# Kernel tuning notes

Hardware: AMD Instinct MI355X
Metric: run time of the kernel (lower is better)

Reference implementation:

```python
import jax, jax.numpy as jnp
import numpy as np

J = 24          # SMPL_NR_JOINTS
H = 24          # hidden_dim
D_IN = 3        # input_dim (xyz)
SMPL_PARENTS = [-1, 0, 0, 0, 1, 2, 3, 4, 5, 6, 7, 8, 9, 9, 9, 12, 13, 14, 16, 17, 18, 19, 20, 21]

def _build_A():
    # undirected kinematic tree + self loops, row-normalized (mean aggregation)
    M = np.zeros((J, J), np.float32)
    for child, parent in enumerate(SMPL_PARENTS):
        if parent >= 0:
            M[child, parent] = 1.0
            M[parent, child] = 1.0
    M += np.eye(J, dtype=np.float32)
    M /= M.sum(axis=1, keepdims=True)
    return jnp.asarray(M)

A_NORM = _build_A()  # [J, J]

def setup_inputs() -> dict:
    key = jax.random.key(0)
    ks = jax.random.split(key, 12)
    B, S, T = 2048, 24, 24
    g = lambda k, shape, s=0.1: jax.random.normal(k, shape, dtype=jnp.float32) * s
    return {
        "src": g(ks[0], (B, S, J, D_IN), 1.0),
        "tgt": g(ks[1], (B, T, J, D_IN), 1.0),
        "We": g(ks[2], (H, D_IN)), "be": jnp.zeros((H,), jnp.float32),
        # gate order: 0=i, 1=f, 2=c, 3=o
        "Wxl": g(ks[3], (4, H, H)), "bxl": jnp.zeros((4, H), jnp.float32),
        "Wxr": g(ks[4], (4, H, H)),
        "Whl": g(ks[5], (4, H, H)), "bhl": jnp.zeros((4, H), jnp.float32),
        "Whr": g(ks[6], (4, H, H)),
        "wg": g(ks[7], (3, H)),   # peephole weights for i, f, o
        "bg": jnp.zeros((4, H), jnp.float32),
        "Wd": g(ks[8], (D_IN * J, H * J)), "bd": jnp.zeros((D_IN * J,), jnp.float32),
    }

def _gconv(x, Wl, bl, Wr):
    # x: [B, J, D]; mean-aggregate over fixed 24-node graph, then l(agg) + r(x)
    agg = jnp.einsum('ij,bjd->bid', A_NORM, x)
    return agg @ Wl.T + bl + x @ Wr.T

def _cell(X, h, c, Wxl, bxl, Wxr, Whl, bhl, Whr, wg, bg):
    gx = lambda g: _gconv(X, Wxl[g], bxl[g], Wxr[g])
    gh = lambda g: _gconv(h, Whl[g], bhl[g], Whr[g])
    i = jax.nn.sigmoid(gx(0) + gh(0) + wg[0] * c + bg[0])
    f = jax.nn.sigmoid(gx(1) + gh(1) + wg[1] * c + bg[1])
    c_new = f * c + i * jnp.tanh(gx(2) + gh(2) + bg[2])
    o = jax.nn.sigmoid(gx(3) + gh(3) + wg[2] * c_new + bg[3])
    h_new = o * jnp.tanh(c_new)
    return o, h_new, c_new

def reference(src, tgt, We, be, Wxl, bxl, Wxr, Whl, bhl, Whr, wg, bg, Wd, bd):
    B, S = src.shape[0], src.shape[1]
    T = tgt.shape[1]
    params = (Wxl, bxl, Wxr, Whl, bhl, Whr, wg, bg)
    enc = lambda x: jax.nn.relu(x @ We.T + be)  # [B, J, H]

    # --- warm-up over last 24 src frames (deterministic: encode only first step) ---
    X0 = enc(src[:, S - 24])
    h = jnp.zeros((B, J, H), src.dtype)
    c = jnp.zeros((B, J, H), src.dtype)
    out, h, c = _cell(X0, h, c, *params)

    def warm_step(carry, _):
        o_, h_, c_ = carry
        o_, h_, c_ = _cell(o_, h_, c_, *params)
        return (o_, h_, c_), None
    (out, h, c), _ = jax.lax.scan(warm_step, (out, h, c), None, length=23)

    # --- decode T steps: first input is enc(tgt[:,0]), then feed previous out ---
    out0, h, c = _cell(enc(tgt[:, 0]), h, c, *params)

    def dec_step(carry, _):
        o_, h_, c_ = carry
        o2, h2, c2 = _cell(o_, h_, c_, *params)
        return (o2, h2, c2), o2
    _, rest = jax.lax.scan(dec_step, (out0, h, c), None, length=T - 1)  # [T-1, B, J, H]

    seq = jnp.concatenate([out0[None], rest], axis=0)            # [T, B, J, H]
    outs = seq.transpose(1, 0, 2, 3).reshape(B, T, J * H)        # [B, T, 576]
    return outs @ Wd.T + bd                                      # [B, T, 72]
```

## Files before the change

kernel.cpp:

```cpp
#include <hip/hip_runtime.h>


typedef short s16x8 __attribute__((ext_vector_type(8)));
typedef float f32x4 __attribute__((ext_vector_type(4)));

#define TPB 192
#define NB 2
#define A_OFF    0
#define G_OFF    19968
#define BIAS_OFF 39552
#define WG_OFF   39936
#define SMEM_SZ  40224

__device__ __forceinline__ float b2f(unsigned short u) {
    return __uint_as_float(((unsigned int)u) << 16);
}
__device__ __forceinline__ unsigned short f2b(float f) {
    unsigned int x = __float_as_uint(f);
    x = x + 0x7fffu + ((x >> 16) & 1u);
    return (unsigned short)(x >> 16);
}
__device__ __forceinline__ unsigned int pk2(float a, float b) {
    return (unsigned int)f2b(a) | ((unsigned int)f2b(b) << 16);
}
__device__ __forceinline__ float frcp(float x) { return __builtin_amdgcn_rcpf(x); }
__device__ __forceinline__ float sigm(float x) {
    float t = __expf(-x);
    return frcp(1.0f + t);
}
__device__ __forceinline__ float tanh_(float x) {
    float xc = fmaxf(x, -30.f);
    float t = __expf(-2.f * xc);
    return (1.f - t) * frcp(1.f + t);
}

extern "C" __global__ void __launch_bounds__(TPB, 3)
gclstm_main(const float* __restrict__ src,
            const float* __restrict__ tgt,
            const float* __restrict__ We,
            const float* __restrict__ be,
            const float* __restrict__ Wxl,
            const float* __restrict__ bxl,
            const float* __restrict__ Wxr,
            const float* __restrict__ Whl,
            const float* __restrict__ bhl,
            const float* __restrict__ Whr,
            const float* __restrict__ wg,
            const float* __restrict__ bg,
            unsigned short* __restrict__ seqh)
{
    __shared__ __align__(16) char smem[SMEM_SZ];
    unsigned short* PQt = (unsigned short*)(smem + A_OFF);
    unsigned short* UO  = (unsigned short*)(smem + A_OFF);
    float* G  = (float*)(smem + G_OFF);
    float* biasL = (float*)(smem + BIAS_OFF);
    float* wgL = (float*)(smem + WG_OFF);

    const int tid = threadIdx.x;
    const int b0 = blockIdx.x * NB;
    const int lane = tid & 63, wid = tid >> 6;
    const int l15 = lane & 15, quad = lane >> 4;

    const int par[24] = {-1,0,0,0,1,2,3,4,5,6,7,8,9,9,9,12,13,14,16,17,18,19,20,21};

    s16x8 w1f[4][2];
#pragma unroll
    for (int cj = 0; cj < 4; ++cj) {
        int np = (wid * 4 + cj) * 16 + l15;
        int path = np >= 96 ? 1 : 0;
        int nn = np - path * 96;
        int g = nn / 24, d = nn - g * 24;
        const float* Wx = path ? Wxr : Wxl;
        const float* Wh = path ? Whr : Whl;
#pragma unroll
        for (int kt = 0; kt < 2; ++kt) {
            s16x8 f;
#pragma unroll
            for (int kk = 0; kk < 8; ++kk) {
                int k = kt * 32 + quad * 8 + kk;
                float v = 0.f;
                if (k < 24) v = Wx[g * 576 + d * 24 + k];
                else if (k < 48) v = Wh[g * 576 + d * 24 + (k - 24)];
                f[kk] = (short)f2b(v);
            }
            w1f[cj][kt] = f;
        }
    }

    s16x8 mf[3][3];
#pragma unroll
    for (int rt = 0; rt < 3; ++rt) {
        int i = rt * 16 + l15;
        int si = i / 24, ji = i - si * 24;
        int cnt = 1 + (par[ji] >= 0 ? 1 : 0);
#pragma unroll
        for (int ch = 0; ch < 24; ++ch) cnt += (par[ch] == ji) ? 1 : 0;
        float cntf = (float)cnt;
#pragma unroll
        for (int kt = 0; kt < 3; ++kt) {
            s16x8 f;
#pragma unroll
            for (int kk = 0; kk < 8; ++kk) {
                int jp = kt * 32 + quad * 8 + kk;
                float v = 0.f;
                if (jp < 48) {
                    int sj = jp / 24, jj = jp - sj * 24;
                    if (sj == si && (jj == ji || par[jj] == ji || par[ji] == jj)) v = 1.f;
                } else {
                    if (jp - 48 == i) v = cntf;
                }
                f[kk] = (short)f2b(v);
            }
            mf[rt][kt] = f;
        }
    }

    if (tid < 96) biasL[tid] = bxl[tid] + bhl[tid] + bg[tid];
    if (tid < 72) wgL[tid] = wg[tid];

    int rowT[3], dpT[3];
    float iwT[3];
    long long seqbT[3];
#pragma unroll
    for (int t = 0; t < 3; ++t) {
        int task = tid + t * TPB;
        int row = task / 12, dp = task - row * 12;
        int j = row % 24;
        rowT[t] = row; dpT[t] = dp;
        int cnt = 1 + (par[j] >= 0 ? 1 : 0);
#pragma unroll
        for (int ch = 0; ch < 24; ++ch) cnt += (par[ch] == j) ? 1 : 0;
        iwT[t] = cnt == 2 ? 0.5f : cnt == 3 ? (1.f / 3.f) : cnt == 4 ? 0.25f : 0.2f;
        seqbT[t] = (long long)(b0 + row / 24) * 24 * 576 + (long long)j * 24 + 2 * dp;
    }

    float creg[3][2];
#pragma unroll
    for (int t = 0; t < 3; ++t) { creg[t][0] = 0.f; creg[t][1] = 0.f; }

#pragma unroll
    for (int t = 0; t < 3; ++t) {
        int row = rowT[t], dp = dpT[t];
        int b = b0 + row / 24, j = row % 24;
        const float* sp = src + (size_t)b * 1728 + j * 3;
        float s0 = sp[0], s1 = sp[1], s2 = sp[2];
        int d = 2 * dp;
        float x0 = be[d] + s0 * We[d * 3] + s1 * We[d * 3 + 1] + s2 * We[d * 3 + 2];
        float x1 = be[d + 1] + s0 * We[d * 3 + 3] + s1 * We[d * 3 + 4] + s2 * We[d * 3 + 5];
        x0 = fmaxf(x0, 0.f); x1 = fmaxf(x1, 0.f);
        *(unsigned int*)(UO + row * 72 + d) = pk2(x0, x1);
        *(unsigned int*)(UO + row * 72 + 24 + d) = 0u;
        *(unsigned int*)(UO + row * 72 + 48 + d) = 0u;
    }
    __syncthreads();

    for (int s = 0; s < 48; ++s) {
        if (s == 24) {
#pragma unroll
            for (int t = 0; t < 3; ++t) {
                int row = rowT[t], dp = dpT[t];
                int b = b0 + row / 24, j = row % 24;
                const float* tp = tgt + (size_t)b * 1728 + j * 3;
                float s0 = tp[0], s1 = tp[1], s2 = tp[2];
                int d = 2 * dp;
                float x0 = be[d] + s0 * We[d * 3] + s1 * We[d * 3 + 1] + s2 * We[d * 3 + 2];
                float x1 = be[d + 1] + s0 * We[d * 3 + 3] + s1 * We[d * 3 + 4]
                         + s2 * We[d * 3 + 5];
                x0 = fmaxf(x0, 0.f); x1 = fmaxf(x1, 0.f);
                *(unsigned int*)(UO + row * 72 + d) = pk2(x0, x1);
            }
            __syncthreads();
        }

        f32x4 acc1[3][4];
#pragma unroll
        for (int rt = 0; rt < 3; ++rt)
#pragma unroll
            for (int cj = 0; cj < 4; ++cj) acc1[rt][cj] = (f32x4)0.f;
#pragma unroll
        for (int kt = 0; kt < 2; ++kt)
#pragma unroll
            for (int rt = 0; rt < 3; ++rt) {
                s16x8 a = *(const s16x8*)(UO + (rt * 16 + l15) * 72 + kt * 32 + quad * 8);
#pragma unroll
                for (int cj = 0; cj < 4; ++cj)
                    acc1[rt][cj] = __builtin_amdgcn_mfma_f32_16x16x32_bf16(a, w1f[cj][kt], acc1[rt][cj], 0, 0, 0);
            }
        __syncthreads();

#pragma unroll
        for (int rt = 0; rt < 3; ++rt)
#pragma unroll
            for (int cj = 0; cj < 4; ++cj) {
                int np = (wid * 4 + cj) * 16 + l15;
                int r96 = np >= 96 ? np - 96 : np;
                int col = (np >= 96 ? 48 : 0) + rt * 16 + quad * 4;
                uint2 wv;
                wv.x = pk2(acc1[rt][cj][0], acc1[rt][cj][1]);
                wv.y = pk2(acc1[rt][cj][2], acc1[rt][cj][3]);
                *(uint2*)(PQt + r96 * 104 + col) = wv;
            }
        __syncthreads();

        f32x4 acc2[3][2];
#pragma unroll
        for (int rt = 0; rt < 3; ++rt)
#pragma unroll
            for (int j2 = 0; j2 < 2; ++j2) acc2[rt][j2] = (f32x4)0.f;
#pragma unroll
        for (int kt = 0; kt < 3; ++kt)
#pragma unroll
            for (int j2 = 0; j2 < 2; ++j2) {
                s16x8 b = *(const s16x8*)(PQt + ((wid * 2 + j2) * 16 + l15) * 104 + kt * 32 + quad * 8);
#pragma unroll
                for (int rt = 0; rt < 3; ++rt) {
                    if (rt == 0 && kt == 2) continue;
                    acc2[rt][j2] = __builtin_amdgcn_mfma_f32_16x16x32_bf16(mf[rt][kt], b, acc2[rt][j2], 0, 0, 0);
                }
            }
#pragma unroll
        for (int rt = 0; rt < 3; ++rt)
#pragma unroll
            for (int j2 = 0; j2 < 2; ++j2) {
                int n = (wid * 2 + j2) * 16 + l15;
                int ib = rt * 16 + quad * 4;
#pragma unroll
                for (int r = 0; r < 4; ++r)
                    G[(ib + r) * 102 + n] = acc2[rt][j2][r];
            }
        __syncthreads();

#pragma unroll
        for (int t = 0; t < 3; ++t) {
            int row = rowT[t], dp = dpT[t];
            float iw = iwT[t];
            const float* Gr = G + row * 102 + 2 * dp;
            float2 gi = *(const float2*)(Gr);
            float2 gf = *(const float2*)(Gr + 24);
            float2 gc = *(const float2*)(Gr + 48);
            float2 go = *(const float2*)(Gr + 72);
            float2 bi = *(const float2*)(biasL + 2 * dp);
            float2 bff = *(const float2*)(biasL + 24 + 2 * dp);
            float2 bcc = *(const float2*)(biasL + 48 + 2 * dp);
            float2 boo = *(const float2*)(biasL + 72 + 2 * dp);
            float2 wi = *(const float2*)(wgL + 2 * dp);
            float2 wf = *(const float2*)(wgL + 24 + 2 * dp);
            float2 wo = *(const float2*)(wgL + 48 + 2 * dp);
            float ov0, ov1, hv0, hv1;
            {
                float c = creg[t][0];
                float pi = fmaf(iw, gi.x, bi.x);
                float pf = fmaf(iw, gf.x, bff.x);
                float pc = fmaf(iw, gc.x, bcc.x);
                float po = fmaf(iw, go.x, boo.x);
                float iv = sigm(fmaf(wi.x, c, pi));
                float fv = sigm(fmaf(wf.x, c, pf));
                float cn = fmaf(fv, c, iv * tanh_(pc));
                float o  = sigm(fmaf(wo.x, cn, po));
                creg[t][0] = cn; ov0 = o; hv0 = o * tanh_(cn);
            }
            {
                float c = creg[t][1];
                float pi = fmaf(iw, gi.y, bi.y);
                float pf = fmaf(iw, gf.y, bff.y);
                float pc = fmaf(iw, gc.y, bcc.y);
                float po = fmaf(iw, go.y, boo.y);
                float iv = sigm(fmaf(wi.y, c, pi));
                float fv = sigm(fmaf(wf.y, c, pf));
                float cn = fmaf(fv, c, iv * tanh_(pc));
                float o  = sigm(fmaf(wo.y, cn, po));
                creg[t][1] = cn; ov1 = o; hv1 = o * tanh_(cn);
            }
            if (s >= 24) {
                long long off = seqbT[t] + (long long)(s - 24) * 576;
                *(unsigned int*)(seqh + off) = pk2(ov0, ov1);
            }
            *(unsigned int*)(UO + row * 72 + 2 * dp) = pk2(ov0, ov1);
            *(unsigned int*)(UO + row * 72 + 24 + 2 * dp) = pk2(hv0, hv1);
            *(unsigned int*)(UO + row * 72 + 48 + 2 * dp) = 0u;
        }
        __syncthreads();
    }
}

extern "C" __global__ void __launch_bounds__(256)
wd_conv(const float* __restrict__ Wd, unsigned short* __restrict__ WdH)
{
    int i = blockIdx.x * 256 + threadIdx.x;
    if (i < 46080) {
        int n = i / 576, k = i - n * 576;
        WdH[i] = (n < 72) ? f2b(Wd[n * 576 + k]) : (unsigned short)0;
    }
}

template <int PRECONV>
__global__ void __launch_bounds__(256, 4)
gclstm_proj(const unsigned short* __restrict__ seqh,
            const unsigned short* __restrict__ WdH,
            const float* __restrict__ Wd,
            const float* __restrict__ bd,
            float* __restrict__ out)
{
    __shared__ unsigned short SQ[64 * 104];
    __shared__ unsigned short WH[80 * 104];

    const int tid = threadIdx.x;
    const int R0 = blockIdx.x * 64;
    const int lane = tid & 63, wid = tid >> 6;
    const int l15 = lane & 15, quad = lane >> 4;

    f32x4 acc[5];
#pragma unroll
    for (int j = 0; j < 5; ++j) acc[j] = (f32x4)0.f;

    if (PRECONV) {
        s16x8 sreg[3], wreg[4];
#pragma unroll
        for (int j = 0; j < 3; ++j) {
            int i = tid + j * 256; int r = i / 12, c8 = i - r * 12;
            sreg[j] = *(const s16x8*)(seqh + (size_t)(R0 + r) * 576 + (size_t)(c8 * 8));
        }
#pragma unroll
        for (int j = 0; j < 4; ++j) {
            int i = tid + j * 256;
            if (i < 960) { int n = i / 12, c8 = i - n * 12;
                wreg[j] = *(const s16x8*)(WdH + (size_t)n * 576 + (size_t)(c8 * 8)); }
        }
        for (int kc = 0; kc < 576; kc += 96) {
#pragma unroll
            for (int j = 0; j < 3; ++j) {
                int i = tid + j * 256; int r = i / 12, c8 = i - r * 12;
                *(s16x8*)(&SQ[r * 104 + c8 * 8]) = sreg[j];
            }
#pragma unroll
            for (int j = 0; j < 4; ++j) {
                int i = tid + j * 256;
                if (i < 960) { int n = i / 12, c8 = i - n * 12;
                    *(s16x8*)(&WH[n * 104 + c8 * 8]) = wreg[j]; }
            }
            __syncthreads();
            if (kc + 96 < 576) {
#pragma unroll
                for (int j = 0; j < 3; ++j) {
                    int i = tid + j * 256; int r = i / 12, c8 = i - r * 12;
                    sreg[j] = *(const s16x8*)(seqh + (size_t)(R0 + r) * 576 + (size_t)(kc + 96 + c8 * 8));
                }
#pragma unroll
                for (int j = 0; j < 4; ++j) {
                    int i = tid + j * 256;
                    if (i < 960) { int n = i / 12, c8 = i - n * 12;
                        wreg[j] = *(const s16x8*)(WdH + (size_t)n * 576 + (size_t)(kc + 96 + c8 * 8)); }
                }
            }
#pragma unroll
            for (int kt = 0; kt < 3; ++kt) {
                int koff = kt * 32 + quad * 8;
                s16x8 a = *(const s16x8*)(&SQ[(wid * 16 + l15) * 104 + koff]);
#pragma unroll
                for (int j = 0; j < 5; ++j) {
                    s16x8 b = *(const s16x8*)(&WH[(j * 16 + l15) * 104 + koff]);
                    acc[j] = __builtin_amdgcn_mfma_f32_16x16x32_bf16(a, b, acc[j], 0, 0, 0);
                }
            }
            __syncthreads();
        }
    } else {
        for (int kc = 0; kc < 576; kc += 96) {
            __syncthreads();
            for (int i = tid; i < 768; i += 256) {
                int r = i / 12, c8 = i - r * 12;
                *(s16x8*)(&SQ[r * 104 + c8 * 8]) =
                    *(const s16x8*)(seqh + (size_t)(R0 + r) * 576 + (size_t)(kc + c8 * 8));
            }
            for (int i = tid; i < 7680; i += 256) {
                int n = i / 96, kk = i - n * 96;
                float v = (n < 72) ? Wd[(size_t)n * 576 + (size_t)(kc + kk)] : 0.f;
                WH[n * 104 + kk] = f2b(v);
            }
            __syncthreads();
#pragma unroll
            for (int kt = 0; kt < 3; ++kt) {
                int koff = kt * 32 + quad * 8;
                s16x8 a = *(const s16x8*)(&SQ[(wid * 16 + l15) * 104 + koff]);
#pragma unroll
                for (int j = 0; j < 5; ++j) {
                    s16x8 b = *(const s16x8*)(&WH[(j * 16 + l15) * 104 + koff]);
                    acc[j] = __builtin_amdgcn_mfma_f32_16x16x32_bf16(a, b, acc[j], 0, 0, 0);
                }
            }
        }
    }

#pragma unroll
    for (int j = 0; j < 5; ++j) {
        int n = j * 16 + l15;
        if (n < 72) {
            float bv = bd[n];
            int rbase = R0 + wid * 16 + quad * 4;
#pragma unroll
            for (int r = 0; r < 4; ++r)
                out[(size_t)(rbase + r) * 72 + (size_t)n] = acc[j][r] + bv;
        }
    }
}

extern "C" void kernel_launch(void* const* d_in, const int* in_sizes, int n_in,
                              void* d_out, int out_size, void* d_ws, size_t ws_size,
                              hipStream_t stream)
{
    const float* src = (const float*)d_in[0];
    const float* tgt = (const float*)d_in[1];
    const float* We  = (const float*)d_in[2];
    const float* be  = (const float*)d_in[3];
    const float* Wxl = (const float*)d_in[4];
    const float* bxl = (const float*)d_in[5];
    const float* Wxr = (const float*)d_in[6];
    const float* Whl = (const float*)d_in[7];
    const float* bhl = (const float*)d_in[8];
    const float* Whr = (const float*)d_in[9];
    const float* wg  = (const float*)d_in[10];
    const float* bg  = (const float*)d_in[11];
    const float* Wd  = (const float*)d_in[12];
    const float* bd  = (const float*)d_in[13];
    float* out = (float*)d_out;
    unsigned short* seqh = (unsigned short*)d_ws;

    const size_t seq_bytes = (size_t)2048 * 24 * 576 * 2;
    unsigned short* WdH = (unsigned short*)((char*)d_ws + seq_bytes);
    const bool preconv = ws_size >= seq_bytes + (size_t)80 * 576 * 2;

    if (preconv)
        wd_conv<<<dim3(180), dim3(256), 0, stream>>>(Wd, WdH);
    gclstm_main<<<dim3(1024), dim3(TPB), 0, stream>>>(
        src, tgt, We, be, Wxl, bxl, Wxr, Whl, bhl, Whr, wg, bg, seqh);
    if (preconv)
        gclstm_proj<1><<<dim3(768), dim3(256), 0, stream>>>(seqh, WdH, Wd, bd, out);
    else
        gclstm_proj<0><<<dim3(768), dim3(256), 0, stream>>>(seqh, nullptr, Wd, bd, out);
}
```

Baseline: 369.9 us.

## Keep graph-aggregation results in registers and fuse gate math via lane shuffles

The second MFMA stage is re-partitioned so each wave owns 16 output rows and all 96 gate columns, so gate pre-activations stay in accumulator registers. The cross-lane shuffles supply the matching gate columns, which removes the fp32 G staging buffer and its barrier. Separate PQ and UO regions also let one barrier after the first GEMM go, and bias and peephole weights now live in registers instead of LDS. In exchange, half the lanes do redundant work on the second hidden slice, and the element-wise writes become 16-bit scattered stores instead of packed pairs.

```diff
diff --git a/kernel.cpp b/kernel.cpp
--- a/kernel.cpp
+++ b/kernel.cpp
@@ -6,15 +6,10 @@
 
 #define TPB 192
 #define NB 2
-#define A_OFF    0
-#define G_OFF    19968
-#define BIAS_OFF 39552
-#define WG_OFF   39936
-#define SMEM_SZ  40224
-
-__device__ __forceinline__ float b2f(unsigned short u) {
-    return __uint_as_float(((unsigned int)u) << 16);
-}
+#define PQ_OFF 0
+#define UO_OFF 19968
+#define SMEM_SZ 26880
+
 __device__ __forceinline__ unsigned short f2b(float f) {
     unsigned int x = __float_as_uint(f);
     x = x + 0x7fffu + ((x >> 16) & 1u);
@@ -50,11 +45,8 @@
             unsigned short* __restrict__ seqh)
 {
     __shared__ __align__(16) char smem[SMEM_SZ];
-    unsigned short* PQt = (unsigned short*)(smem + A_OFF);
-    unsigned short* UO  = (unsigned short*)(smem + A_OFF);
-    float* G  = (float*)(smem + G_OFF);
-    float* biasL = (float*)(smem + BIAS_OFF);
-    float* wgL = (float*)(smem + WG_OFF);
+    unsigned short* PQt = (unsigned short*)(smem + PQ_OFF);
+    unsigned short* UO  = (unsigned short*)(smem + UO_OFF);
 
     const int tid = threadIdx.x;
     const int b0 = blockIdx.x * NB;
@@ -87,10 +79,9 @@
         }
     }
 
-    s16x8 mf[3][3];
-#pragma unroll
-    for (int rt = 0; rt < 3; ++rt) {
-        int i = rt * 16 + l15;
+    s16x8 mf[3];
+    {
+        int i = wid * 16 + l15;
         int si = i / 24, ji = i - si * 24;
         int cnt = 1 + (par[ji] >= 0 ? 1 : 0);
 #pragma unroll
@@ -111,36 +102,43 @@
                 }
                 f[kk] = (short)f2b(v);
             }
-            mf[rt][kt] = f;
-        }
-    }
-
-    if (tid < 96) biasL[tid] = bxl[tid] + bhl[tid] + bg[tid];
-    if (tid < 72) wgL[tid] = wg[tid];
-
-    int rowT[3], dpT[3];
-    float iwT[3];
-    long long seqbT[3];
+            mf[kt] = f;
+        }
+    }
+
+    const int d1 = l15;
+    const int d2 = 16 + (l15 & 7);
+    float bC1[4], bC2[4], wv1[3], wv2[3];
+#pragma unroll
+    for (int g = 0; g < 4; ++g) {
+        bC1[g] = bxl[g * 24 + d1] + bhl[g * 24 + d1] + bg[g * 24 + d1];
+        bC2[g] = bxl[g * 24 + d2] + bhl[g * 24 + d2] + bg[g * 24 + d2];
+    }
+#pragma unroll
+    for (int p = 0; p < 3; ++p) { wv1[p] = wg[p * 24 + d1]; wv2[p] = wg[p * 24 + d2]; }
+
+    int rowR[4];
+    float iwR[4];
+    long long sb[4];
+#pragma unroll
+    for (int rr = 0; rr < 4; ++rr) {
+        int row = wid * 16 + quad * 4 + rr;
+        rowR[rr] = row;
+        int j = row % 24;
+        int cnt = 1 + (par[j] >= 0 ? 1 : 0);
+#pragma unroll
+        for (int ch = 0; ch < 24; ++ch) cnt += (par[ch] == j) ? 1 : 0;
+        iwR[rr] = cnt == 2 ? 0.5f : cnt == 3 ? (1.f / 3.f) : cnt == 4 ? 0.25f : 0.2f;
+        sb[rr] = (long long)(b0 + row / 24) * 13824 + (long long)j * 24;
+    }
+
+    float c1[4] = {0.f, 0.f, 0.f, 0.f};
+    float c2[2] = {0.f, 0.f};
+
 #pragma unroll
     for (int t = 0; t < 3; ++t) {
         int task = tid + t * TPB;
         int row = task / 12, dp = task - row * 12;
-        int j = row % 24;
-        rowT[t] = row; dpT[t] = dp;
-        int cnt = 1 + (par[j] >= 0 ? 1 : 0);
-#pragma unroll
-        for (int ch = 0; ch < 24; ++ch) cnt += (par[ch] == j) ? 1 : 0;
-        iwT[t] = cnt == 2 ? 0.5f : cnt == 3 ? (1.f / 3.f) : cnt == 4 ? 0.25f : 0.2f;
-        seqbT[t] = (long long)(b0 + row / 24) * 24 * 576 + (long long)j * 24 + 2 * dp;
-    }
-
-    float creg[3][2];
-#pragma unroll
-    for (int t = 0; t < 3; ++t) { creg[t][0] = 0.f; creg[t][1] = 0.f; }
-
-#pragma unroll
-    for (int t = 0; t < 3; ++t) {
-        int row = rowT[t], dp = dpT[t];
         int b = b0 + row / 24, j = row % 24;
         const float* sp = src + (size_t)b * 1728 + j * 3;
         float s0 = sp[0], s1 = sp[1], s2 = sp[2];
@@ -158,7 +156,8 @@
         if (s == 24) {
 #pragma unroll
             for (int t = 0; t < 3; ++t) {
-                int row = rowT[t], dp = dpT[t];
+                int task = tid + t * TPB;
+                int row = task / 12, dp = task - row * 12;
                 int b = b0 + row / 24, j = row % 24;
                 const float* tp = tgt + (size_t)b * 1728 + j * 3;
                 float s0 = tp[0], s1 = tp[1], s2 = tp[2];
@@ -178,16 +177,17 @@
 #pragma unroll
             for (int cj = 0; cj < 4; ++cj) acc1[rt][cj] = (f32x4)0.f;
 #pragma unroll
-        for (int kt = 0; kt < 2; ++kt)
-#pragma unroll
-            for (int rt = 0; rt < 3; ++rt) {
-                s16x8 a = *(const s16x8*)(UO + (rt * 16 + l15) * 72 + kt * 32 + quad * 8);
+        for (int kt = 0; kt < 2; ++kt) {
+            s16x8 a[3];
+#pragma unroll
+            for (int rt = 0; rt < 3; ++rt)
+                a[rt] = *(const s16x8*)(UO + (rt * 16 + l15) * 72 + kt * 32 + quad * 8);
+#pragma unroll
+            for (int rt = 0; rt < 3; ++rt)
 #pragma unroll
                 for (int cj = 0; cj < 4; ++cj)
-                    acc1[rt][cj] = __builtin_amdgcn_mfma_f32_16x16x32_bf16(a, w1f[cj][kt], acc1[rt][cj], 0, 0, 0);
-            }
-        __syncthreads();
-
+                    acc1[rt][cj] = __builtin_amdgcn_mfma_f32_16x16x32_bf16(a[rt], w1f[cj][kt], acc1[rt][cj], 0, 0, 0);
+        }
 #pragma unroll
         for (int rt = 0; rt < 3; ++rt)
 #pragma unroll
@@ -202,82 +202,72 @@
             }
         __syncthreads();
 
-        f32x4 acc2[3][2];
-#pragma unroll
-        for (int rt = 0; rt < 3; ++rt)
-#pragma unroll
-            for (int j2 = 0; j2 < 2; ++j2) acc2[rt][j2] = (f32x4)0.f;
-#pragma unroll
-        for (int kt = 0; kt < 3; ++kt)
-#pragma unroll
-            for (int j2 = 0; j2 < 2; ++j2) {
-                s16x8 b = *(const s16x8*)(PQt + ((wid * 2 + j2) * 16 + l15) * 104 + kt * 32 + quad * 8);
-#pragma unroll
-                for (int rt = 0; rt < 3; ++rt) {
-                    if (rt == 0 && kt == 2) continue;
-                    acc2[rt][j2] = __builtin_amdgcn_mfma_f32_16x16x32_bf16(mf[rt][kt], b, acc2[rt][j2], 0, 0, 0);
-                }
-            }
-#pragma unroll
-        for (int rt = 0; rt < 3; ++rt)
-#pragma unroll
-            for (int j2 = 0; j2 < 2; ++j2) {
-                int n = (wid * 2 + j2) * 16 + l15;
-                int ib = rt * 16 + quad * 4;
-#pragma unroll
-                for (int r = 0; r < 4; ++r)
-                    G[(ib + r) * 102 + n] = acc2[rt][j2][r];
-            }
-        __syncthreads();
-
-#pragma unroll
-        for (int t = 0; t < 3; ++t) {
-            int row = rowT[t], dp = dpT[t];
-            float iw = iwT[t];
-            const float* Gr = G + row * 102 + 2 * dp;
-            float2 gi = *(const float2*)(Gr);
-            float2 gf = *(const float2*)(Gr + 24);
-            float2 gc = *(const float2*)(Gr + 48);
-            float2 go = *(const float2*)(Gr + 72);
-            float2 bi = *(const float2*)(biasL + 2 * dp);
-            float2 bff = *(const float2*)(biasL + 24 + 2 * dp);
-            float2 bcc = *(const float2*)(biasL + 48 + 2 * dp);
-            float2 boo = *(const float2*)(biasL + 72 + 2 * dp);
-            float2 wi = *(const float2*)(wgL + 2 * dp);
-            float2 wf = *(const float2*)(wgL + 24 + 2 * dp);
-            float2 wo = *(const float2*)(wgL + 48 + 2 * dp);
-            float ov0, ov1, hv0, hv1;
+        f32x4 acc2[6];
+#pragma unroll
+        for (int nt = 0; nt < 6; ++nt) acc2[nt] = (f32x4)0.f;
+#pragma unroll
+        for (int kt = 0; kt < 3; ++kt) {
+            if (kt == 2 && wid == 0) continue;
+            s16x8 bf[6];
+#pragma unroll
+            for (int nt = 0; nt < 6; ++nt)
+                bf[nt] = *(const s16x8*)(PQt + (nt * 16 + l15) * 104 + kt * 32 + quad * 8);
+#pragma unroll
+            for (int nt = 0; nt < 6; ++nt)
+                acc2[nt] = __builtin_amdgcn_mfma_f32_16x16x32_bf16(mf[kt], bf[nt], acc2[nt], 0, 0, 0);
+        }
+
+        const bool lo = l15 < 8;
+#pragma unroll
+        for (int rr = 0; rr < 4; ++rr) {
+            float a0 = acc2[0][rr], a1 = acc2[1][rr], a2 = acc2[2][rr];
+            float a3 = acc2[3][rr], a4 = acc2[4][rr], a5 = acc2[5][rr];
+            float x1 = __shfl_xor(a1, 8);
+            float x2 = __shfl_xor(a2, 8);
+            float x4 = __shfl_xor(a4, 8);
+            float x5 = __shfl_xor(a5, 8);
+            float iw = iwR[rr];
+            int row = rowR[rr];
             {
-                float c = creg[t][0];
-                float pi = fmaf(iw, gi.x, bi.x);
-                float pf = fmaf(iw, gf.x, bff.x);
-                float pc = fmaf(iw, gc.x, bcc.x);
-                float po = fmaf(iw, go.x, boo.x);
-                float iv = sigm(fmaf(wi.x, c, pi));
-                float fv = sigm(fmaf(wf.x, c, pf));
+                float c = c1[rr];
+                float pi = fmaf(iw, a0, bC1[0]);
+                float pf = fmaf(iw, lo ? x1 : x2, bC1[1]);
+                float pc = fmaf(iw, a3, bC1[2]);
+                float po = fmaf(iw, lo ? x4 : x5, bC1[3]);
+                float iv = sigm(fmaf(wv1[0], c, pi));
+                float fv = sigm(fmaf(wv1[1], c, pf));
                 float cn = fmaf(fv, c, iv * tanh_(pc));
-                float o  = sigm(fmaf(wo.x, cn, po));
-                creg[t][0] = cn; ov0 = o; hv0 = o * tanh_(cn);
+                float ov = sigm(fmaf(wv1[2], cn, po));
+                c1[rr] = cn;
+                float hv = ov * tanh_(cn);
+                UO[row * 72 + d1] = f2b(ov);
+                UO[row * 72 + 24 + d1] = f2b(hv);
+                if (s >= 24) seqh[sb[rr] + (long long)(s - 24) * 576 + d1] = f2b(ov);
             }
             {
-                float c = creg[t][1];
-                float pi = fmaf(iw, gi.y, bi.y);
-                float pf = fmaf(iw, gf.y, bff.y);
-                float pc = fmaf(iw, gc.y, bcc.y);
-                float po = fmaf(iw, go.y, boo.y);
-                float iv = sigm(fmaf(wi.y, c, pi));
-                float fv = sigm(fmaf(wf.y, c, pf));
+                const bool schemeA = (rr < 2);
+                bool act = schemeA ? lo : !lo;
+                float g0 = schemeA ? a1 : x1;
+                float g1 = schemeA ? x2 : a2;
+                float g2 = schemeA ? a4 : x4;
+                float g3 = schemeA ? x5 : a5;
+                float c = c2[rr & 1];
+                float pi = fmaf(iw, g0, bC2[0]);
+                float pf = fmaf(iw, g1, bC2[1]);
+                float pc = fmaf(iw, g2, bC2[2]);
+                float po = fmaf(iw, g3, bC2[3]);
+                float iv = sigm(fmaf(wv2[0], c, pi));
+                float fv = sigm(fmaf(wv2[1], c, pf));
                 float cn = fmaf(fv, c, iv * tanh_(pc));
-                float o  = sigm(fmaf(wo.y, cn, po));
-                creg[t][1] = cn; ov1 = o; hv1 = o * tanh_(cn);
-            }
-            if (s >= 24) {
-                long long off = seqbT[t] + (long long)(s - 24) * 576;
-                *(unsigned int*)(seqh + off) = pk2(ov0, ov1);
-            }
-            *(unsigned int*)(UO + row * 72 + 2 * dp) = pk2(ov0, ov1);
-            *(unsigned int*)(UO + row * 72 + 24 + 2 * dp) = pk2(hv0, hv1);
-            *(unsigned int*)(UO + row * 72 + 48 + 2 * dp) = 0u;
+                float ov = sigm(fmaf(wv2[2], cn, po));
+                float hv = ov * tanh_(cn);
+                if (act) {
+                    c2[rr & 1] = cn;
+                    UO[row * 72 + d2] = f2b(ov);
+                    UO[row * 72 + 24 + d2] = f2b(hv);
+                    if (s >= 24) seqh[sb[rr] + (long long)(s - 24) * 576 + d2] = f2b(ov);
+                }
+            }
         }
         __syncthreads();
     }
```

Result: no change. 376.9 us (+1.9%).
